# Performance work log

Hardware: AMD Instinct MI355X
Metric: run time of the kernel (lower is better)

The kernel has to match this reference:

```python
import jax, jax.numpy as jnp
import numpy as np

B, T, H = 32, 1000, 512


def setup_inputs() -> dict:
    key = jax.random.key(0)
    k1, k2, k3, k4, k5 = jax.random.split(key, 5)
    return {
        "wx": jax.random.normal(k1, (B, T, 4 * H), dtype=jnp.float32),
        "u": jax.random.normal(k2, (4 * H, H), dtype=jnp.float32) * (1.0 / np.sqrt(H)),
        "u_bias": jax.random.normal(k3, (4 * H,), dtype=jnp.float32) * 0.1,
        "ht": jax.random.normal(k4, (B, H), dtype=jnp.float32),
        "ct": jax.random.normal(k5, (B, H), dtype=jnp.float32),
    }


def reference(wx, u, u_bias, ht, ct):
    # wx: [B, T, 4H]; scan over time with sequential (ht, ct) state.
    def step(carry, wx_t):
        h, c = carry
        gates = wx_t + h @ u.T + u_bias          # [B, 4H]
        it, ft, gt, ot = jnp.split(gates, 4, axis=1)
        it = jax.nn.sigmoid(it)
        ft = jax.nn.sigmoid(ft)
        gt = jnp.tanh(gt)
        ot = jax.nn.sigmoid(ot)
        c = ft * c + it * gt
        h = ot * jnp.tanh(c)
        return (h, c), (h, c, it, ft, gt, ot)

    wx_t = jnp.swapaxes(wx, 0, 1)                # [T, B, 4H]
    _, (h, c, it, ft, gt, ot) = jax.lax.scan(step, (ht, ct), wx_t)
    # each is [T, B, H] -> [B, T, H]
    tr = lambda a: jnp.swapaxes(a, 0, 1)
    return tr(h), tr(c), tr(it), tr(ft), tr(gt), tr(ot)
```

## Files before the change

### kernel.cpp

```cpp
#include <hip/hip_runtime.h>

#define BB 32
#define TT 1000
#define HH 512
#define G4 2048
#define BTH ((size_t)BB * TT * HH)

typedef short short8 __attribute__((ext_vector_type(8)));
typedef float f32x4 __attribute__((ext_vector_type(4)));

__device__ __forceinline__ unsigned short f2bf(float f) {
    union { float f; unsigned u; } v; v.f = f;
    unsigned r = v.u + 0x7FFF + ((v.u >> 16) & 1);
    return (unsigned short)(r >> 16);
}

#define RING_WORDS (2 * 8 * 32 * 64)

__global__ void lstm_init_ring(unsigned* ring) {
    int i = blockIdx.x * 256 + threadIdx.x;
    __hip_atomic_store(ring + i, 0xFFFFFFFFu, __ATOMIC_RELAXED,
                       __HIP_MEMORY_SCOPE_AGENT);
}

__global__ void __launch_bounds__(256, 1)
lstm_main(const float* __restrict__ wx, const float* __restrict__ u,
          const float* __restrict__ ub, const float* __restrict__ ht0,
          const float* __restrict__ ct0, float* __restrict__ out,
          unsigned* __restrict__ ring)
{
    __shared__ __align__(16) unsigned short lds_h[16 * 512];
    __shared__ float lds_gates[4 * 64];

    const int tid  = threadIdx.x;
    const int bid  = blockIdx.x;
    const int cg   = bid & 31;
    const int qb   = bid >> 5;
    const int lane = tid & 63;
    const int wv   = tid >> 6;

    for (int j = 0; j < 3; ++j) {
        int idx8 = tid + j * 256;
        int r = 4 + (idx8 >> 6);
        int k = (idx8 & 63) * 8;
        short8 z = {0, 0, 0, 0, 0, 0, 0, 0};
        *(short8*)&lds_h[(r * 512 + k) ^ ((r & 7) << 3)] = z;
    }
    {
        int r = wv;
        int k = lane * 8;
        const float* src = ht0 + (size_t)(qb * 4 + r) * HH + k;
        float4 v0 = *(const float4*)src;
        float4 v1 = *(const float4*)(src + 4);
        union { short8 v8; unsigned short s[8]; } p;
        p.s[0] = f2bf(v0.x); p.s[1] = f2bf(v0.y); p.s[2] = f2bf(v0.z); p.s[3] = f2bf(v0.w);
        p.s[4] = f2bf(v1.x); p.s[5] = f2bf(v1.y); p.s[6] = f2bf(v1.z); p.s[7] = f2bf(v1.w);
        *(short8*)&lds_h[(r * 512 + k) ^ ((r & 7) << 3)] = p.v8;
    }

    const int arow = lane & 15, ahi = lane >> 4;
    short8 breg[16];
    {
        const float* bp = u + (size_t)(wv * HH + cg * 16 + arow) * HH + ahi * 8;
#pragma unroll
        for (int kk = 0; kk < 16; ++kk) {
            float4 v0 = *(const float4*)(bp + kk * 32);
            float4 v1 = *(const float4*)(bp + kk * 32 + 4);
            union { short8 v8; unsigned short s[8]; } p;
            p.s[0] = f2bf(v0.x); p.s[1] = f2bf(v0.y); p.s[2] = f2bf(v0.z); p.s[3] = f2bf(v0.w);
            p.s[4] = f2bf(v1.x); p.s[5] = f2bf(v1.y); p.s[6] = f2bf(v1.z); p.s[7] = f2bf(v1.w);
            breg[kk] = p.v8;
        }
    }

    const int gate = lane >> 4;
    const int jc   = lane & 15;
    const float bias_r = ub[gate * HH + cg * 16 + jc];

    float c_reg = 0.f;
    if (lane < 16)
        c_reg = ct0[(size_t)(qb * 4 + wv) * HH + cg * 16 + lane];

    const size_t wx0 = (size_t)(qb * 4 + wv) * TT * G4 + gate * HH + cg * 16 + jc;
    float wx_cur = wx[wx0];
    float wx_nxt = wx[wx0 + G4];

    const size_t ob_gate = (size_t)(2 + gate) * BTH +
                           (size_t)(qb * 4 + wv) * TT * HH + cg * 16 + jc;
    const size_t ob_h = (size_t)(qb * 4 + wv) * TT * HH + cg * 16 + lane;

    const int a_off = arow * 512 + ahi * 8;
    const int a_msk = (arow & 7) << 3;

    const int myp = tid >> 3;
    const int mw  = (tid & 7) * 8;
    const int mb  = mw >> 4;
    const int mj  = mw & 15;

    __syncthreads();

    for (int t = 0; t < TT; ++t) {
        if (t > 0 && myp != cg) {
            const unsigned long long* src = (const unsigned long long*)
                (ring + ((size_t)((t - 1) & 1) * 8 + qb) * 2048 + myp * 64 + mw);
            const unsigned tg = (unsigned)((t - 1) & 0xFFFF);
            const unsigned long long want =
                (unsigned long long)tg | ((unsigned long long)tg << 32);
            const unsigned long long msk = 0x0000FFFF0000FFFFull;
            unsigned long long q0, q1, q2, q3;
            for (;;) {
                q0 = __hip_atomic_load(src + 0, __ATOMIC_RELAXED, __HIP_MEMORY_SCOPE_AGENT);
                q1 = __hip_atomic_load(src + 1, __ATOMIC_RELAXED, __HIP_MEMORY_SCOPE_AGENT);
                q2 = __hip_atomic_load(src + 2, __ATOMIC_RELAXED, __HIP_MEMORY_SCOPE_AGENT);
                q3 = __hip_atomic_load(src + 3, __ATOMIC_RELAXED, __HIP_MEMORY_SCOPE_AGENT);
                if (((q0 & msk) == want) & ((q1 & msk) == want) &
                    ((q2 & msk) == want) & ((q3 & msk) == want)) break;
            }
            union { short8 v8; unsigned u[4]; } pv;
            pv.u[0] = ((unsigned)(q0 >> 16) & 0xFFFFu) | ((unsigned)(q0 >> 48) << 16);
            pv.u[1] = ((unsigned)(q1 >> 16) & 0xFFFFu) | ((unsigned)(q1 >> 48) << 16);
            pv.u[2] = ((unsigned)(q2 >> 16) & 0xFFFFu) | ((unsigned)(q2 >> 48) << 16);
            pv.u[3] = ((unsigned)(q3 >> 16) & 0xFFFFu) | ((unsigned)(q3 >> 48) << 16);
            *(short8*)&lds_h[(mb * 512 + myp * 16 + mj) ^ ((mb & 7) << 3)] = pv.v8;
        }
        __syncthreads();

        const float wx_use = wx_cur;
        wx_cur = wx_nxt;
        if (t + 2 < TT) wx_nxt = wx[wx0 + (size_t)(t + 2) * G4];

        f32x4 acc0 = {0.f, 0.f, 0.f, 0.f}, acc1 = {0.f, 0.f, 0.f, 0.f};
#pragma unroll
        for (int kk = 0; kk < 8; ++kk) {
            short8 a0 = *(const short8*)&lds_h[(a_off + kk * 32) ^ a_msk];
            short8 a1 = *(const short8*)&lds_h[(a_off + (kk + 8) * 32) ^ a_msk];
            acc0 = __builtin_amdgcn_mfma_f32_16x16x32_bf16(a0, breg[kk], acc0, 0, 0, 0);
            acc1 = __builtin_amdgcn_mfma_f32_16x16x32_bf16(a1, breg[kk + 8], acc1, 0, 0, 0);
        }
        f32x4 g = acc0 + acc1;
        if (lane < 16) {
#pragma unroll
            for (int rr = 0; rr < 4; ++rr)
                lds_gates[rr * 64 + wv * 16 + lane] = g[rr];
        }
        __syncthreads();

        float gv = lds_gates[wv * 64 + lane] + wx_use + bias_r;
        float xs = (gate == 2) ? 2.f * gv : gv;
        float s  = 1.f / (1.f + __expf(-xs));
        float act = (gate == 2) ? 2.f * s - 1.f : s;

        float af = __shfl(act, (lane & 15) + 16, 64);
        float ag = __shfl(act, (lane & 15) + 32, 64);
        float ao = __shfl(act, (lane & 15) + 48, 64);
        if (lane < 16) {
            c_reg = af * c_reg + act * ag;
            float e2 = __expf(-2.f * c_reg);
            float th = 2.f / (1.f + e2) - 1.f;
            float hn = ao * th;
            unsigned short hb = f2bf(hn);
            unsigned pk = ((unsigned)hb << 16) | (unsigned)(t & 0xFFFF);
            __hip_atomic_store(ring + ((size_t)(t & 1) * 8 + qb) * 2048 +
                                   cg * 64 + wv * 16 + lane,
                               pk, __ATOMIC_RELAXED, __HIP_MEMORY_SCOPE_AGENT);
            lds_h[(wv * 512 + cg * 16 + lane) ^ ((wv & 7) << 3)] = hb;
            out[ob_h + (size_t)t * HH] = hn;
            out[BTH + ob_h + (size_t)t * HH] = c_reg;
        }
        out[ob_gate + (size_t)t * HH] = act;
    }
}

extern "C" void kernel_launch(void* const* d_in, const int* in_sizes, int n_in,
                              void* d_out, int out_size, void* d_ws, size_t ws_size,
                              hipStream_t stream) {
    const float* wx = (const float*)d_in[0];
    const float* u  = (const float*)d_in[1];
    const float* ub = (const float*)d_in[2];
    const float* ht = (const float*)d_in[3];
    const float* ct = (const float*)d_in[4];
    float* out = (float*)d_out;
    unsigned* ring = (unsigned*)d_ws;

    lstm_init_ring<<<RING_WORDS / 256, 256, 0, stream>>>(ring);

    void* args[] = {(void*)&wx, (void*)&u, (void*)&ub, (void*)&ht,
                    (void*)&ct, (void*)&out, (void*)&ring};
    hipLaunchCooperativeKernel((void*)lstm_main, dim3(256), dim3(256), args, 0, stream);
}
```

Before: 1.702 ms.

## Interleave gates within each wave and double-buffer LDS to drop a barrier

Each wave's MFMA tile now covers all four gates for 4 hidden columns instead of one gate for 16 columns. The gate combination can then be done with in-wave shuffles, which removes the lds_gates exchange and the second __syncthreads per timestep. The h buffer in LDS is double-buffered by timestep parity, and local h values are written at the start of the next step so the single barrier is enough. In exchange, fewer lanes do the elementwise work (16 lanes compute activations, 4 lanes update the cell state), output stores become narrower and strided, and the wx prefetch is reshaped.

```diff
diff --git a/kernel.cpp b/kernel.cpp
--- a/kernel.cpp
+++ b/kernel.cpp
@@ -29,8 +29,7 @@
           const float* __restrict__ ct0, float* __restrict__ out,
           unsigned* __restrict__ ring)
 {
-    __shared__ __align__(16) unsigned short lds_h[16 * 512];
-    __shared__ float lds_gates[4 * 64];
+    __shared__ __align__(16) unsigned short lds_h[2][16 * 512];
 
     const int tid  = threadIdx.x;
     const int bid  = blockIdx.x;
@@ -38,30 +37,35 @@
     const int qb   = bid >> 5;
     const int lane = tid & 63;
     const int wv   = tid >> 6;
-
-    for (int j = 0; j < 3; ++j) {
+    const int c    = lane & 15;
+    const int ahi  = lane >> 4;
+    const int gate = c >> 2;
+    const int jj   = c & 3;
+    const int jcol = wv * 4 + jj;
+
+    for (int j = 0; j < 6; ++j) {
         int idx8 = tid + j * 256;
-        int r = 4 + (idx8 >> 6);
-        int k = (idx8 & 63) * 8;
+        int buf  = idx8 >= 768;
+        int r8   = idx8 - buf * 768;
+        int r    = 4 + (r8 >> 6);
+        int k    = (r8 & 63) * 8;
         short8 z = {0, 0, 0, 0, 0, 0, 0, 0};
-        *(short8*)&lds_h[(r * 512 + k) ^ ((r & 7) << 3)] = z;
+        *(short8*)&lds_h[buf][(r * 512 + k) ^ ((r & 7) << 3)] = z;
     }
     {
-        int r = wv;
-        int k = lane * 8;
+        int r = wv, k = lane * 8;
         const float* src = ht0 + (size_t)(qb * 4 + r) * HH + k;
         float4 v0 = *(const float4*)src;
         float4 v1 = *(const float4*)(src + 4);
         union { short8 v8; unsigned short s[8]; } p;
         p.s[0] = f2bf(v0.x); p.s[1] = f2bf(v0.y); p.s[2] = f2bf(v0.z); p.s[3] = f2bf(v0.w);
         p.s[4] = f2bf(v1.x); p.s[5] = f2bf(v1.y); p.s[6] = f2bf(v1.z); p.s[7] = f2bf(v1.w);
-        *(short8*)&lds_h[(r * 512 + k) ^ ((r & 7) << 3)] = p.v8;
-    }
-
-    const int arow = lane & 15, ahi = lane >> 4;
+        *(short8*)&lds_h[0][(r * 512 + k) ^ ((r & 7) << 3)] = p.v8;
+    }
+
     short8 breg[16];
     {
-        const float* bp = u + (size_t)(wv * HH + cg * 16 + arow) * HH + ahi * 8;
+        const float* bp = u + (size_t)(gate * HH + cg * 16 + jcol) * HH + ahi * 8;
 #pragma unroll
         for (int kk = 0; kk < 16; ++kk) {
             float4 v0 = *(const float4*)(bp + kk * 32);
@@ -73,101 +77,136 @@
         }
     }
 
-    const int gate = lane >> 4;
-    const int jc   = lane & 15;
-    const float bias_r = ub[gate * HH + cg * 16 + jc];
-
-    float c_reg = 0.f;
-    if (lane < 16)
-        c_reg = ct0[(size_t)(qb * 4 + wv) * HH + cg * 16 + lane];
-
-    const size_t wx0 = (size_t)(qb * 4 + wv) * TT * G4 + gate * HH + cg * 16 + jc;
-    float wx_cur = wx[wx0];
-    float wx_nxt = wx[wx0 + G4];
-
-    const size_t ob_gate = (size_t)(2 + gate) * BTH +
-                           (size_t)(qb * 4 + wv) * TT * HH + cg * 16 + jc;
-    const size_t ob_h = (size_t)(qb * 4 + wv) * TT * HH + cg * 16 + lane;
-
-    const int a_off = arow * 512 + ahi * 8;
-    const int a_msk = (arow & 7) << 3;
+    const float bias_r = ub[gate * HH + cg * 16 + jcol];
+
+    float c_reg[4];
+#pragma unroll
+    for (int rr = 0; rr < 4; ++rr)
+        c_reg[rr] = ct0[(size_t)(qb * 4 + rr) * HH + cg * 16 + jcol];
+
+    size_t wx0[4];
+    size_t ob_act[4], ob_h[4];
+#pragma unroll
+    for (int rr = 0; rr < 4; ++rr) {
+        wx0[rr]    = (size_t)(qb * 4 + rr) * TT * G4 + gate * HH + cg * 16 + jcol;
+        ob_act[rr] = (size_t)(2 + gate) * BTH +
+                     (size_t)(qb * 4 + rr) * TT * HH + cg * 16 + jcol;
+        ob_h[rr]   = (size_t)(qb * 4 + rr) * TT * HH + cg * 16 + jcol;
+    }
+    float wx_cur[4] = {0, 0, 0, 0}, wx_nxt[4] = {0, 0, 0, 0}, wx_tmp[4] = {0, 0, 0, 0};
+    if (lane < 16) {
+#pragma unroll
+        for (int rr = 0; rr < 4; ++rr) {
+            wx_cur[rr] = wx[wx0[rr]];
+            wx_nxt[rr] = wx[wx0[rr] + G4];
+        }
+    }
+
+    const int a_off = c * 512 + ahi * 8;
+    const int a_msk = (c & 7) << 3;
 
     const int myp = tid >> 3;
     const int mw  = (tid & 7) * 8;
     const int mb  = mw >> 4;
     const int mj  = mw & 15;
 
+    unsigned short hb[4] = {0, 0, 0, 0};
+
     __syncthreads();
 
     for (int t = 0; t < TT; ++t) {
-        if (t > 0 && myp != cg) {
-            const unsigned long long* src = (const unsigned long long*)
-                (ring + ((size_t)((t - 1) & 1) * 8 + qb) * 2048 + myp * 64 + mw);
-            const unsigned tg = (unsigned)((t - 1) & 0xFFFF);
-            const unsigned long long want =
-                (unsigned long long)tg | ((unsigned long long)tg << 32);
-            const unsigned long long msk = 0x0000FFFF0000FFFFull;
-            unsigned long long q0, q1, q2, q3;
-            for (;;) {
-                q0 = __hip_atomic_load(src + 0, __ATOMIC_RELAXED, __HIP_MEMORY_SCOPE_AGENT);
-                q1 = __hip_atomic_load(src + 1, __ATOMIC_RELAXED, __HIP_MEMORY_SCOPE_AGENT);
-                q2 = __hip_atomic_load(src + 2, __ATOMIC_RELAXED, __HIP_MEMORY_SCOPE_AGENT);
-                q3 = __hip_atomic_load(src + 3, __ATOMIC_RELAXED, __HIP_MEMORY_SCOPE_AGENT);
-                if (((q0 & msk) == want) & ((q1 & msk) == want) &
-                    ((q2 & msk) == want) & ((q3 & msk) == want)) break;
-            }
-            union { short8 v8; unsigned u[4]; } pv;
-            pv.u[0] = ((unsigned)(q0 >> 16) & 0xFFFFu) | ((unsigned)(q0 >> 48) << 16);
-            pv.u[1] = ((unsigned)(q1 >> 16) & 0xFFFFu) | ((unsigned)(q1 >> 48) << 16);
-            pv.u[2] = ((unsigned)(q2 >> 16) & 0xFFFFu) | ((unsigned)(q2 >> 48) << 16);
-            pv.u[3] = ((unsigned)(q3 >> 16) & 0xFFFFu) | ((unsigned)(q3 >> 48) << 16);
-            *(short8*)&lds_h[(mb * 512 + myp * 16 + mj) ^ ((mb & 7) << 3)] = pv.v8;
+        const int cur = t & 1;
+
+        if (lane < 16 && t + 2 < TT) {
+#pragma unroll
+            for (int rr = 0; rr < 4; ++rr)
+                wx_tmp[rr] = wx[wx0[rr] + (size_t)(t + 2) * G4];
+        }
+
+        if (t > 0) {
+            if (lane < 4) {
+#pragma unroll
+                for (int rr = 0; rr < 4; ++rr)
+                    lds_h[cur][(rr * 512 + cg * 16 + jcol) ^ (rr << 3)] = hb[rr];
+            }
+            if (myp != cg) {
+                const unsigned long long* src = (const unsigned long long*)
+                    (ring + ((size_t)(cur ^ 1) * 8 + qb) * 2048 + myp * 64 + mw);
+                const unsigned tg = (unsigned)(t - 1);
+                const unsigned long long want =
+                    (unsigned long long)tg | ((unsigned long long)tg << 32);
+                const unsigned long long msk = 0x0000FFFF0000FFFFull;
+                unsigned long long q0, q1, q2, q3;
+                for (;;) {
+                    q0 = __hip_atomic_load(src + 0, __ATOMIC_RELAXED, __HIP_MEMORY_SCOPE_AGENT);
+                    q1 = __hip_atomic_load(src + 1, __ATOMIC_RELAXED, __HIP_MEMORY_SCOPE_AGENT);
+                    q2 = __hip_atomic_load(src + 2, __ATOMIC_RELAXED, __HIP_MEMORY_SCOPE_AGENT);
+                    q3 = __hip_atomic_load(src + 3, __ATOMIC_RELAXED, __HIP_MEMORY_SCOPE_AGENT);
+                    if (((q0 & msk) == want) & ((q1 & msk) == want) &
+                        ((q2 & msk) == want) & ((q3 & msk) == want)) break;
+                }
+                union { short8 v8; unsigned u[4]; } pv;
+                pv.u[0] = ((unsigned)(q0 >> 16) & 0xFFFFu) | ((unsigned)(q0 >> 48) << 16);
+                pv.u[1] = ((unsigned)(q1 >> 16) & 0xFFFFu) | ((unsigned)(q1 >> 48) << 16);
+                pv.u[2] = ((unsigned)(q2 >> 16) & 0xFFFFu) | ((unsigned)(q2 >> 48) << 16);
+                pv.u[3] = ((unsigned)(q3 >> 16) & 0xFFFFu) | ((unsigned)(q3 >> 48) << 16);
+                *(short8*)&lds_h[cur][(mb * 512 + myp * 16 + mj) ^ ((mb & 7) << 3)] = pv.v8;
+            }
         }
         __syncthreads();
 
-        const float wx_use = wx_cur;
-        wx_cur = wx_nxt;
-        if (t + 2 < TT) wx_nxt = wx[wx0 + (size_t)(t + 2) * G4];
-
         f32x4 acc0 = {0.f, 0.f, 0.f, 0.f}, acc1 = {0.f, 0.f, 0.f, 0.f};
 #pragma unroll
         for (int kk = 0; kk < 8; ++kk) {
-            short8 a0 = *(const short8*)&lds_h[(a_off + kk * 32) ^ a_msk];
-            short8 a1 = *(const short8*)&lds_h[(a_off + (kk + 8) * 32) ^ a_msk];
-            acc0 = __builtin_amdgcn_mfma_f32_16x16x32_bf16(a0, breg[kk], acc0, 0, 0, 0);
-            acc1 = __builtin_amdgcn_mfma_f32_16x16x32_bf16(a1, breg[kk + 8], acc1, 0, 0, 0);
+            short8 va0 = *(const short8*)&lds_h[cur][(a_off + kk * 32) ^ a_msk];
+            short8 va1 = *(const short8*)&lds_h[cur][(a_off + (kk + 8) * 32) ^ a_msk];
+            acc0 = __builtin_amdgcn_mfma_f32_16x16x32_bf16(va0, breg[kk], acc0, 0, 0, 0);
+            acc1 = __builtin_amdgcn_mfma_f32_16x16x32_bf16(va1, breg[kk + 8], acc1, 0, 0, 0);
         }
         f32x4 g = acc0 + acc1;
+
         if (lane < 16) {
+            float act[4];
+#pragma unroll
+            for (int rr = 0; rr < 4; ++rr) {
+                float gv = g[rr] + wx_cur[rr] + bias_r;
+                float xs = (gate == 2) ? 2.f * gv : gv;
+                float s  = 1.f / (1.f + __expf(-xs));
+                act[rr]  = (gate == 2) ? 2.f * s - 1.f : s;
+            }
+            float af[4], ag[4], ao[4];
+#pragma unroll
+            for (int rr = 0; rr < 4; ++rr) {
+                af[rr] = __shfl(act[rr], 4 + jj, 64);
+                ag[rr] = __shfl(act[rr], 8 + jj, 64);
+                ao[rr] = __shfl(act[rr], 12 + jj, 64);
+            }
+            if (lane < 4) {
+#pragma unroll
+                for (int rr = 0; rr < 4; ++rr) {
+                    c_reg[rr] = af[rr] * c_reg[rr] + act[rr] * ag[rr];
+                    float e2 = __expf(-2.f * c_reg[rr]);
+                    float th = 2.f / (1.f + e2) - 1.f;
+                    float hn = ao[rr] * th;
+                    hb[rr] = f2bf(hn);
+                    unsigned pk = ((unsigned)hb[rr] << 16) | (unsigned)t;
+                    __hip_atomic_store(ring + ((size_t)cur * 8 + qb) * 2048 +
+                                           cg * 64 + rr * 16 + jcol,
+                                       pk, __ATOMIC_RELAXED, __HIP_MEMORY_SCOPE_AGENT);
+                    out[ob_h[rr] + (size_t)t * HH] = hn;
+                    out[BTH + ob_h[rr] + (size_t)t * HH] = c_reg[rr];
+                }
+            }
 #pragma unroll
             for (int rr = 0; rr < 4; ++rr)
-                lds_gates[rr * 64 + wv * 16 + lane] = g[rr];
-        }
-        __syncthreads();
-
-        float gv = lds_gates[wv * 64 + lane] + wx_use + bias_r;
-        float xs = (gate == 2) ? 2.f * gv : gv;
-        float s  = 1.f / (1.f + __expf(-xs));
-        float act = (gate == 2) ? 2.f * s - 1.f : s;
-
-        float af = __shfl(act, (lane & 15) + 16, 64);
-        float ag = __shfl(act, (lane & 15) + 32, 64);
-        float ao = __shfl(act, (lane & 15) + 48, 64);
-        if (lane < 16) {
-            c_reg = af * c_reg + act * ag;
-            float e2 = __expf(-2.f * c_reg);
-            float th = 2.f / (1.f + e2) - 1.f;
-            float hn = ao * th;
-            unsigned short hb = f2bf(hn);
-            unsigned pk = ((unsigned)hb << 16) | (unsigned)(t & 0xFFFF);
-            __hip_atomic_store(ring + ((size_t)(t & 1) * 8 + qb) * 2048 +
-                                   cg * 64 + wv * 16 + lane,
-                               pk, __ATOMIC_RELAXED, __HIP_MEMORY_SCOPE_AGENT);
-            lds_h[(wv * 512 + cg * 16 + lane) ^ ((wv & 7) << 3)] = hb;
-            out[ob_h + (size_t)t * HH] = hn;
-            out[BTH + ob_h + (size_t)t * HH] = c_reg;
-        }
-        out[ob_gate + (size_t)t * HH] = act;
+                out[ob_act[rr] + (size_t)t * HH] = act[rr];
+        }
+
+#pragma unroll
+        for (int rr = 0; rr < 4; ++rr) {
+            wx_cur[rr] = wx_nxt[rr];
+            wx_nxt[rr] = wx_tmp[rr];
+        }
     }
 }
 
```

Result: slower. 2.355 ms (+38.4%).
